# Kernel optimization log

Measured on AMD Instinct MI355X. Metric: run time of the kernel, lower is better.

Reference implementation:

```python
import jax, jax.numpy as jnp
import numpy as np

DIM = 512
N_GROUPS = 8
N_CODES = 1024
SUB = DIM // N_GROUPS
CB_LAMBDA = 1.0
COMMIT_LAMBDA = 0.25


def setup_inputs() -> dict:
    key = jax.random.key(0)
    k1, k2, k3 = jax.random.split(key, 3)
    x = jax.random.normal(k1, (8, DIM, 4096), dtype=jnp.float32)
    lim = 1.0 / N_CODES
    codebooks1 = jax.random.uniform(k2, (N_GROUPS, N_CODES, SUB), dtype=jnp.float32, minval=-lim, maxval=lim)
    codebooks2 = jax.random.uniform(k3, (N_GROUPS, N_CODES, SUB), dtype=jnp.float32, minval=-lim, maxval=lim)
    return {"x": x, "codebooks1": codebooks1, "codebooks2": codebooks2}


def _quantize_group(flat, cbs):
    # flat: (N, G, d), cbs: (G, K, d)
    x2 = jnp.sum(flat * flat, axis=-1, keepdims=True)          # (N, G, 1)
    e2 = jnp.sum(cbs * cbs, axis=-1)                            # (G, K)
    xe = jnp.einsum('ngd,gkd->ngk', flat, cbs)                  # (N, G, K)
    d = x2 + e2[None, :, :] - 2.0 * xe                          # (N, G, K)
    idx = jnp.argmin(d, axis=-1)                                # (N, G)
    z = cbs[jnp.arange(N_GROUPS)[None, :], idx]                 # (N, G, d)
    return z, idx


def reference(x, codebooks1, codebooks2):
    B, C, T = x.shape
    sg = jax.lax.stop_gradient
    # (B, C, T) -> (B*T, G, sub)
    xb = jnp.transpose(x, (0, 2, 1)).reshape(-1, N_GROUPS, SUB)
    residual = xb
    quantized = jnp.zeros_like(xb)
    losses = []
    all_indices = []
    for cbs in (codebooks1, codebooks2):
        z, idx = _quantize_group(residual, cbs)
        codebook_loss = jnp.mean((z - sg(residual)) ** 2)
        commit_loss = jnp.mean((sg(z) - residual) ** 2)
        losses.append(CB_LAMBDA * codebook_loss + COMMIT_LAMBDA * commit_loss)
        z_st = residual + sg(z - residual)  # straight-through
        residual = residual - z_st
        quantized = quantized + z_st
        all_indices.append(idx)
    total_loss = jnp.mean(jnp.stack(losses))
    quantized_out = jnp.transpose(quantized.reshape(B, T, C), (0, 2, 1))
    # indices in original order: layer-major, group-major -> (layers*G, B*T)
    indices = jnp.concatenate([idx.T for idx in all_indices], axis=0)
    return quantized_out, total_loss, indices
```

## Files before the change

### kernel.cpp

```cpp
#include <hip/hip_runtime.h>

#define GRP 8
#define SUBD 64
#define NCODE 1024
#define TLEN 4096
#define NBATCH 8
#define NVEC (NBATCH * TLEN)
#define QOUT (NBATCH * 512 * TLEN)
#define ROWS 128
#define NGRPS (NCODE / 8)

#define WS_E2   64
#define WS_IDX1 (WS_E2 + 65536)
#define WS_P1   (WS_IDX1 + 1048576)
#define WS_P2   (WS_P1 + 2097152)

typedef const __attribute__((address_space(1))) char GCHAR;
typedef __attribute__((address_space(3))) char LCHAR;
typedef float f2 __attribute__((ext_vector_type(2)));

__global__ __launch_bounds__(256) void k_e2(const float* __restrict__ cb1,
                                            const float* __restrict__ cb2,
                                            float* __restrict__ e2) {
    int i = blockIdx.x * 256 + threadIdx.x;
    const float* c = (i < GRP * NCODE) ? (cb1 + (size_t)i * SUBD)
                                       : (cb2 + (size_t)(i - GRP * NCODE) * SUBD);
    float s = 0.f;
#pragma unroll
    for (int d = 0; d < SUBD; ++d) s = __builtin_fmaf(c[d], c[d], s);
    e2[i] = s;
}

__global__ __launch_bounds__(256) void k_panel(const float* __restrict__ cb1,
                                               const float* __restrict__ cb2,
                                               float* __restrict__ cbP1,
                                               float* __restrict__ cbP2) {
    int i = blockIdx.x * 256 + threadIdx.x;
    int sel = i >> 13, rest = i & 8191, g = rest >> 10, k = rest & 1023;
    int grp = k >> 3, j = k & 7;
    const float* src = (sel ? cb2 : cb1) + ((size_t)g * NCODE + k) * SUBD;
    float* dst = (sel ? cbP2 : cbP1) + ((size_t)(g * NGRPS + grp) * SUBD) * 8 + j;
#pragma unroll
    for (int s = 0; s < 16; ++s) {
        float4 v = ((const float4*)src)[s];
#pragma unroll
        for (int dd = 0; dd < 4; ++dd) dst[(4 * s + dd) * 8] = ((const float*)&v)[dd];
    }
}

template <int STAGE2>
__global__ __launch_bounds__(256, 3) void k_vq(
    const float* __restrict__ x,
    const float* __restrict__ cb1,
    const float* __restrict__ cb2,
    const float* __restrict__ cbP,
    const float* __restrict__ e2,
    const int* __restrict__ idxPrev,
    int* __restrict__ idxOut,
    float* __restrict__ outIdxF,
    float* __restrict__ qout,
    double* __restrict__ lossAcc)
{
    __shared__ __align__(16) float xs[SUBD * ROWS];
    __shared__ float bdH[4 * ROWS];
    __shared__ int   biH[4 * ROWS];
    __shared__ int   i2s[ROWS];
    __shared__ double wsr[8];

    const int tid = threadIdx.x, w = tid >> 6, lane = tid & 63;
    const int g = blockIdx.y;
    const int row0 = blockIdx.x * ROWS;
    const int bz = row0 / TLEN, t0 = row0 % TLEN;
    const float* xsrc = x + ((size_t)(bz * 512 + g * SUBD)) * TLEN + t0;

    {
#pragma unroll
        for (int q = 0; q < 8; ++q) {
            int inst = w * 8 + q;
            int d = inst * 2 + (lane >> 5);
            const float* gp = xsrc + (size_t)d * TLEN + (lane & 31) * 4;
            float* lp = xs + inst * 256;
            __builtin_amdgcn_global_load_lds((GCHAR*)gp, (LCHAR*)lp, 16, 0, 0);
        }
    }
    __syncthreads();

    const int rowB = tid & 127, hi = tid >> 7;
    double ls1 = 0.0;
    int i1 = 0;
    if (STAGE2) {
        i1 = idxPrev[g * NVEC + row0 + rowB];
        const float4* z1v = (const float4*)(cb1 + ((size_t)g * NCODE + i1) * SUBD) + hi * 8;
#pragma unroll
        for (int s = 0; s < 8; ++s) {
            float4 z = z1v[s];
#pragma unroll
            for (int dd = 0; dd < 4; ++dd) {
                int d = hi * 32 + s * 4 + dd;
                float r = xs[d * ROWS + rowB];
                float zz = (&z.x)[dd];
                float tt = zz - r;
                float zst = r + tt;
                ls1 += (double)(tt * tt);
                float r2 = r - zst;
                xs[d * ROWS + rowB] = r2;
            }
        }
        __syncthreads();
    }

    const int w_u = __builtin_amdgcn_readfirstlane(w);
    const f2* xs2 = (const f2*)xs;

    f2 x2p = {0.f, 0.f};
#pragma unroll 8
    for (int d = 0; d < SUBD; ++d) {
        f2 rv = xs2[d * 64 + lane];
        x2p = __builtin_elementwise_fma(rv, rv, x2p);
    }
    const float x2a = x2p[0], x2b = x2p[1];

    const float* e2g = e2 + g * NCODE;
    float best[2] = {1e30f, 1e30f};
    int bidx[2] = {0, 0};

    for (int ib = 0; ib < 8; ++ib) {
        const float* cp = cbP + ((size_t)(g * NGRPS) + w_u * 32 + ib * 4) * (SUBD * 8);
        const float4* cb0 = (const float4*)(cp);
        const float4* cb1p = (const float4*)(cp + 1 * (SUBD * 8));
        const float4* cb2p = (const float4*)(cp + 2 * (SUBD * 8));
        const float4* cb3p = (const float4*)(cp + 3 * (SUBD * 8));
        f2 acc[2][4][4];
#pragma unroll
        for (int r = 0; r < 2; ++r)
#pragma unroll
            for (int gg = 0; gg < 4; ++gg)
#pragma unroll
                for (int p = 0; p < 4; ++p) acc[r][gg][p] = (f2){0.f, 0.f};

#pragma unroll 2
        for (int d = 0; d < SUBD; ++d) {
            f2 rv = xs2[d * 64 + lane];
            f2 xa2 = {rv[0], rv[0]}, xb2 = {rv[1], rv[1]};
            const float4* cbs[4] = {cb0, cb1p, cb2p, cb3p};
#pragma unroll
            for (int gg = 0; gg < 4; ++gg) {
                float4 q0 = cbs[gg][2 * d];
                float4 q1 = cbs[gg][2 * d + 1];
                f2 cv0 = {q0.x, q0.y}, cv1 = {q0.z, q0.w};
                f2 cv2 = {q1.x, q1.y}, cv3 = {q1.z, q1.w};
                acc[0][gg][0] = __builtin_elementwise_fma(xa2, cv0, acc[0][gg][0]);
                acc[0][gg][1] = __builtin_elementwise_fma(xa2, cv1, acc[0][gg][1]);
                acc[0][gg][2] = __builtin_elementwise_fma(xa2, cv2, acc[0][gg][2]);
                acc[0][gg][3] = __builtin_elementwise_fma(xa2, cv3, acc[0][gg][3]);
                acc[1][gg][0] = __builtin_elementwise_fma(xb2, cv0, acc[1][gg][0]);
                acc[1][gg][1] = __builtin_elementwise_fma(xb2, cv1, acc[1][gg][1]);
                acc[1][gg][2] = __builtin_elementwise_fma(xb2, cv2, acc[1][gg][2]);
                acc[1][gg][3] = __builtin_elementwise_fma(xb2, cv3, acc[1][gg][3]);
            }
        }

#pragma unroll
        for (int gg = 0; gg < 4; ++gg) {
            const float4* e4 = (const float4*)(e2g + w_u * 256 + ib * 32 + gg * 8);
            float4 e0 = e4[0], e1 = e4[1];
#pragma unroll
            for (int p = 0; p < 4; ++p) {
#pragma unroll
                for (int h = 0; h < 2; ++h) {
                    int j = 2 * p + h;
                    int k = w_u * 256 + ib * 32 + gg * 8 + j;
                    float ev = (j < 4) ? (&e0.x)[j] : (&e1.x)[j - 4];
                    float tva = x2a + ev;
                    float da = __builtin_fmaf(-2.0f, acc[0][gg][p][h], tva);
                    if (da < best[0]) { best[0] = da; bidx[0] = k; }
                    float tvb = x2b + ev;
                    float db = __builtin_fmaf(-2.0f, acc[1][gg][p][h], tvb);
                    if (db < best[1]) { best[1] = db; bidx[1] = k; }
                }
            }
        }
    }
    bdH[w * ROWS + 2 * lane]     = best[0];
    biH[w * ROWS + 2 * lane]     = bidx[0];
    bdH[w * ROWS + 2 * lane + 1] = best[1];
    biH[w * ROWS + 2 * lane + 1] = bidx[1];
    __syncthreads();

    if (tid < ROWS) {
        float bd = bdH[tid];
        int   bi = biH[tid];
#pragma unroll
        for (int wv = 1; wv < 4; ++wv) {
            float od = bdH[wv * ROWS + tid];
            int   oi = biH[wv * ROWS + tid];
            if (od < bd) { bd = od; bi = oi; }
        }
        int nv = row0 + tid;
        outIdxF[(size_t)g * NVEC + nv] = (float)bi;
        if (!STAGE2) idxOut[g * NVEC + nv] = bi;
        else i2s[tid] = bi;
    }

    double ls2 = 0.0;
    if (STAGE2) {
        __syncthreads();
        int bi = i2s[rowB];
        const float4* z1v = (const float4*)(cb1 + ((size_t)g * NCODE + i1) * SUBD) + hi * 8;
        const float4* z2v = (const float4*)(cb2 + ((size_t)g * NCODE + bi) * SUBD) + hi * 8;
        const float* xp = xsrc + rowB;
        float* op = qout + ((size_t)(bz * 512 + g * SUBD)) * TLEN + t0 + rowB;
#pragma unroll
        for (int s = 0; s < 8; ++s) {
            float4 z1 = z1v[s];
            float4 z2 = z2v[s];
#pragma unroll
            for (int dd = 0; dd < 4; ++dd) {
                int d = hi * 32 + s * 4 + dd;
                float xv = xp[(size_t)d * TLEN];
                float r2 = xs[d * ROWS + rowB];
                float z1f = (&z1.x)[dd];
                float z2f = (&z2.x)[dd];
                float t1 = z1f - xv;
                float zst1 = xv + t1;
                float t2 = z2f - r2;
                float zst2 = r2 + t2;
                float qv = zst1 + zst2;
                op[(size_t)d * TLEN] = qv;
                ls2 += (double)(t2 * t2);
            }
        }

#pragma unroll
        for (int off = 32; off; off >>= 1) {
            ls1 += __shfl_down(ls1, off, 64);
            ls2 += __shfl_down(ls2, off, 64);
        }
        if (lane == 0) { wsr[w] = ls1; wsr[4 + w] = ls2; }
        __syncthreads();
        if (tid == 0)
            atomicAdd(lossAcc + 0, wsr[0] + wsr[1] + wsr[2] + wsr[3]);
        else if (tid == 64)
            atomicAdd(lossAcc + 1, wsr[4] + wsr[5] + wsr[6] + wsr[7]);
    }
}

__global__ void k_final(float* __restrict__ lossOut, const double* __restrict__ lossAcc) {
    double m = (lossAcc[0] + lossAcc[1]) / (double)QOUT;
    lossOut[0] = (float)(0.625 * m);
}

extern "C" void kernel_launch(void* const* d_in, const int* in_sizes, int n_in,
                              void* d_out, int out_size, void* d_ws, size_t ws_size,
                              hipStream_t stream) {
    const float* x   = (const float*)d_in[0];
    const float* cb1 = (const float*)d_in[1];
    const float* cb2 = (const float*)d_in[2];
    float* out = (float*)d_out;

    char* ws = (char*)d_ws;
    double* lossAcc = (double*)ws;
    float* e2   = (float*)(ws + WS_E2);
    int*   idx1 = (int*)(ws + WS_IDX1);
    float* cbP1 = (float*)(ws + WS_P1);
    float* cbP2 = (float*)(ws + WS_P2);

    hipMemsetAsync(ws, 0, 16, stream);

    k_e2<<<dim3(64), dim3(256), 0, stream>>>(cb1, cb2, e2);
    k_panel<<<dim3(64), dim3(256), 0, stream>>>(cb1, cb2, cbP1, cbP2);

    dim3 grid(NVEC / ROWS, GRP);
    float* outIdx = out + QOUT + 1;
    k_vq<0><<<grid, dim3(256), 0, stream>>>(x, cb1, cb2, cbP1, e2,
                                            nullptr, idx1, outIdx, nullptr, nullptr);
    k_vq<1><<<grid, dim3(256), 0, stream>>>(x, cb1, cb2, cbP2, e2 + GRP * NCODE,
                                            idx1, nullptr, outIdx + (size_t)GRP * NVEC,
                                            out, lossAcc);
    k_final<<<1, 1, 0, stream>>>(out + QOUT, lossAcc);
}
```

Baseline: 795.2 us.

## Double rows per VQ block to 256 with 512 threads sharing codebook panels

Each VQ block now handles 256 rows with 8 waves. Two row-halves of waves scan the same codebook quarters, so each codebook panel fetch from global/L2 is reused across twice as many rows. The x tile load, LDS indexing, per-quarter min reduction and loss reduction are rewritten for the larger block. LDS use per block doubles and the grid halves, which can cut occupancy and the number of blocks available to fill the GPU.

```diff
diff --git a/kernel.cpp b/kernel.cpp
--- a/kernel.cpp
+++ b/kernel.cpp
@@ -7,7 +7,7 @@
 #define NBATCH 8
 #define NVEC (NBATCH * TLEN)
 #define QOUT (NBATCH * 512 * TLEN)
-#define ROWS 128
+#define ROWS 256
 #define NGRPS (NCODE / 8)
 
 #define WS_E2   64
@@ -49,7 +49,7 @@
 }
 
 template <int STAGE2>
-__global__ __launch_bounds__(256, 3) void k_vq(
+__global__ __launch_bounds__(512, 2) void k_vq(
     const float* __restrict__ x,
     const float* __restrict__ cb1,
     const float* __restrict__ cb2,
@@ -65,7 +65,7 @@
     __shared__ float bdH[4 * ROWS];
     __shared__ int   biH[4 * ROWS];
     __shared__ int   i2s[ROWS];
-    __shared__ double wsr[8];
+    __shared__ double wsr[16];
 
     const int tid = threadIdx.x, w = tid >> 6, lane = tid & 63;
     const int g = blockIdx.y;
@@ -75,17 +75,16 @@
 
     {
 #pragma unroll
-        for (int q = 0; q < 8; ++q) {
-            int inst = w * 8 + q;
-            int d = inst * 2 + (lane >> 5);
-            const float* gp = xsrc + (size_t)d * TLEN + (lane & 31) * 4;
-            float* lp = xs + inst * 256;
+        for (int qq = 0; qq < 8; ++qq) {
+            int d = w * 8 + qq;
+            const float* gp = xsrc + (size_t)d * TLEN + lane * 4;
+            float* lp = xs + d * 256;
             __builtin_amdgcn_global_load_lds((GCHAR*)gp, (LCHAR*)lp, 16, 0, 0);
         }
     }
     __syncthreads();
 
-    const int rowB = tid & 127, hi = tid >> 7;
+    const int rowB = tid & 255, hi = tid >> 8;
     double ls1 = 0.0;
     int i1 = 0;
     if (STAGE2) {
@@ -110,12 +109,14 @@
     }
 
     const int w_u = __builtin_amdgcn_readfirstlane(w);
+    const int h = w_u >> 2, q = w_u & 3;
+    const int pr = h * 64 + lane;
     const f2* xs2 = (const f2*)xs;
 
     f2 x2p = {0.f, 0.f};
 #pragma unroll 8
     for (int d = 0; d < SUBD; ++d) {
-        f2 rv = xs2[d * 64 + lane];
+        f2 rv = xs2[d * 128 + pr];
         x2p = __builtin_elementwise_fma(rv, rv, x2p);
     }
     const float x2a = x2p[0], x2b = x2p[1];
@@ -125,11 +126,11 @@
     int bidx[2] = {0, 0};
 
     for (int ib = 0; ib < 8; ++ib) {
-        const float* cp = cbP + ((size_t)(g * NGRPS) + w_u * 32 + ib * 4) * (SUBD * 8);
-        const float4* cb0 = (const float4*)(cp);
-        const float4* cb1p = (const float4*)(cp + 1 * (SUBD * 8));
-        const float4* cb2p = (const float4*)(cp + 2 * (SUBD * 8));
-        const float4* cb3p = (const float4*)(cp + 3 * (SUBD * 8));
+        const float* cp = cbP + ((size_t)(g * NGRPS) + q * 32 + ib * 4) * (SUBD * 8);
+        const float4* cbq0 = (const float4*)(cp);
+        const float4* cbq1 = (const float4*)(cp + 1 * (SUBD * 8));
+        const float4* cbq2 = (const float4*)(cp + 2 * (SUBD * 8));
+        const float4* cbq3 = (const float4*)(cp + 3 * (SUBD * 8));
         f2 acc[2][4][4];
 #pragma unroll
         for (int r = 0; r < 2; ++r)
@@ -140,9 +141,9 @@
 
 #pragma unroll 2
         for (int d = 0; d < SUBD; ++d) {
-            f2 rv = xs2[d * 64 + lane];
+            f2 rv = xs2[d * 128 + pr];
             f2 xa2 = {rv[0], rv[0]}, xb2 = {rv[1], rv[1]};
-            const float4* cbs[4] = {cb0, cb1p, cb2p, cb3p};
+            const float4* cbs[4] = {cbq0, cbq1, cbq2, cbq3};
 #pragma unroll
             for (int gg = 0; gg < 4; ++gg) {
                 float4 q0 = cbs[gg][2 * d];
@@ -162,38 +163,38 @@
 
 #pragma unroll
         for (int gg = 0; gg < 4; ++gg) {
-            const float4* e4 = (const float4*)(e2g + w_u * 256 + ib * 32 + gg * 8);
+            const float4* e4 = (const float4*)(e2g + q * 256 + ib * 32 + gg * 8);
             float4 e0 = e4[0], e1 = e4[1];
 #pragma unroll
             for (int p = 0; p < 4; ++p) {
 #pragma unroll
-                for (int h = 0; h < 2; ++h) {
-                    int j = 2 * p + h;
-                    int k = w_u * 256 + ib * 32 + gg * 8 + j;
+                for (int hh = 0; hh < 2; ++hh) {
+                    int j = 2 * p + hh;
+                    int k = q * 256 + ib * 32 + gg * 8 + j;
                     float ev = (j < 4) ? (&e0.x)[j] : (&e1.x)[j - 4];
                     float tva = x2a + ev;
-                    float da = __builtin_fmaf(-2.0f, acc[0][gg][p][h], tva);
+                    float da = __builtin_fmaf(-2.0f, acc[0][gg][p][hh], tva);
                     if (da < best[0]) { best[0] = da; bidx[0] = k; }
                     float tvb = x2b + ev;
-                    float db = __builtin_fmaf(-2.0f, acc[1][gg][p][h], tvb);
+                    float db = __builtin_fmaf(-2.0f, acc[1][gg][p][hh], tvb);
                     if (db < best[1]) { best[1] = db; bidx[1] = k; }
                 }
             }
         }
     }
-    bdH[w * ROWS + 2 * lane]     = best[0];
-    biH[w * ROWS + 2 * lane]     = bidx[0];
-    bdH[w * ROWS + 2 * lane + 1] = best[1];
-    biH[w * ROWS + 2 * lane + 1] = bidx[1];
+    bdH[q * ROWS + 2 * pr]     = best[0];
+    biH[q * ROWS + 2 * pr]     = bidx[0];
+    bdH[q * ROWS + 2 * pr + 1] = best[1];
+    biH[q * ROWS + 2 * pr + 1] = bidx[1];
     __syncthreads();
 
     if (tid < ROWS) {
         float bd = bdH[tid];
         int   bi = biH[tid];
 #pragma unroll
-        for (int wv = 1; wv < 4; ++wv) {
-            float od = bdH[wv * ROWS + tid];
-            int   oi = biH[wv * ROWS + tid];
+        for (int qv = 1; qv < 4; ++qv) {
+            float od = bdH[qv * ROWS + tid];
+            int   oi = biH[qv * ROWS + tid];
             if (od < bd) { bd = od; bi = oi; }
         }
         int nv = row0 + tid;
@@ -225,8 +226,8 @@
                 float zst1 = xv + t1;
                 float t2 = z2f - r2;
                 float zst2 = r2 + t2;
-                float qv = zst1 + zst2;
-                op[(size_t)d * TLEN] = qv;
+                float qv2 = zst1 + zst2;
+                op[(size_t)d * TLEN] = qv2;
                 ls2 += (double)(t2 * t2);
             }
         }
@@ -236,12 +237,19 @@
             ls1 += __shfl_down(ls1, off, 64);
             ls2 += __shfl_down(ls2, off, 64);
         }
-        if (lane == 0) { wsr[w] = ls1; wsr[4 + w] = ls2; }
+        if (lane == 0) { wsr[w] = ls1; wsr[8 + w] = ls2; }
         __syncthreads();
-        if (tid == 0)
-            atomicAdd(lossAcc + 0, wsr[0] + wsr[1] + wsr[2] + wsr[3]);
-        else if (tid == 64)
-            atomicAdd(lossAcc + 1, wsr[4] + wsr[5] + wsr[6] + wsr[7]);
+        if (tid == 0) {
+            double s = 0.0;
+#pragma unroll
+            for (int i = 0; i < 8; ++i) s += wsr[i];
+            atomicAdd(lossAcc + 0, s);
+        } else if (tid == 64) {
+            double s = 0.0;
+#pragma unroll
+            for (int i = 0; i < 8; ++i) s += wsr[8 + i];
+            atomicAdd(lossAcc + 1, s);
+        }
     }
 }
 
@@ -272,9 +280,9 @@
 
     dim3 grid(NVEC / ROWS, GRP);
     float* outIdx = out + QOUT + 1;
-    k_vq<0><<<grid, dim3(256), 0, stream>>>(x, cb1, cb2, cbP1, e2,
+    k_vq<0><<<grid, dim3(512), 0, stream>>>(x, cb1, cb2, cbP1, e2,
                                             nullptr, idx1, outIdx, nullptr, nullptr);
-    k_vq<1><<<grid, dim3(256), 0, stream>>>(x, cb1, cb2, cbP2, e2 + GRP * NCODE,
+    k_vq<1><<<grid, dim3(512), 0, stream>>>(x, cb1, cb2, cbP2, e2 + GRP * NCODE,
                                             idx1, nullptr, outIdx + (size_t)GRP * NVEC,
                                             out, lossAcc);
     k_final<<<1, 1, 0, stream>>>(out + QOUT, lossAcc);
```

After: 851.5 us. 1.07x slower.

## Fuse both VQ stages into one kernel and merge codebook prep kernels

Applied to the files above, without the earlier changes.

Both residual quantization stages now run in a single kernel. The residual stays in shared memory between stages instead of x being reloaded and stage-1 indices going through global memory. The e2 norm and panel-layout prep kernels are merged into one launch. This removes one full read of x, the idx round trip and two launches. The cost is a longer kernel with extra barriers, and register pressure may change.

```diff
diff --git a/kernel.cpp b/kernel.cpp
--- a/kernel.cpp
+++ b/kernel.cpp
@@ -11,107 +11,43 @@
 #define NGRPS (NCODE / 8)
 
 #define WS_E2   64
-#define WS_IDX1 (WS_E2 + 65536)
-#define WS_P1   (WS_IDX1 + 1048576)
+#define WS_P1   (WS_E2 + 65536)
 #define WS_P2   (WS_P1 + 2097152)
 
 typedef const __attribute__((address_space(1))) char GCHAR;
 typedef __attribute__((address_space(3))) char LCHAR;
 typedef float f2 __attribute__((ext_vector_type(2)));
 
-__global__ __launch_bounds__(256) void k_e2(const float* __restrict__ cb1,
-                                            const float* __restrict__ cb2,
-                                            float* __restrict__ e2) {
-    int i = blockIdx.x * 256 + threadIdx.x;
-    const float* c = (i < GRP * NCODE) ? (cb1 + (size_t)i * SUBD)
-                                       : (cb2 + (size_t)(i - GRP * NCODE) * SUBD);
-    float s = 0.f;
-#pragma unroll
-    for (int d = 0; d < SUBD; ++d) s = __builtin_fmaf(c[d], c[d], s);
-    e2[i] = s;
-}
-
-__global__ __launch_bounds__(256) void k_panel(const float* __restrict__ cb1,
-                                               const float* __restrict__ cb2,
-                                               float* __restrict__ cbP1,
-                                               float* __restrict__ cbP2) {
+__global__ __launch_bounds__(256) void k_prep(const float* __restrict__ cb1,
+                                              const float* __restrict__ cb2,
+                                              float* __restrict__ e2,
+                                              float* __restrict__ cbP1,
+                                              float* __restrict__ cbP2) {
     int i = blockIdx.x * 256 + threadIdx.x;
     int sel = i >> 13, rest = i & 8191, g = rest >> 10, k = rest & 1023;
     int grp = k >> 3, j = k & 7;
     const float* src = (sel ? cb2 : cb1) + ((size_t)g * NCODE + k) * SUBD;
     float* dst = (sel ? cbP2 : cbP1) + ((size_t)(g * NGRPS + grp) * SUBD) * 8 + j;
-#pragma unroll
-    for (int s = 0; s < 16; ++s) {
-        float4 v = ((const float4*)src)[s];
-#pragma unroll
-        for (int dd = 0; dd < 4; ++dd) dst[(4 * s + dd) * 8] = ((const float*)&v)[dd];
-    }
-}
-
-template <int STAGE2>
-__global__ __launch_bounds__(256, 3) void k_vq(
-    const float* __restrict__ x,
-    const float* __restrict__ cb1,
-    const float* __restrict__ cb2,
-    const float* __restrict__ cbP,
-    const float* __restrict__ e2,
-    const int* __restrict__ idxPrev,
-    int* __restrict__ idxOut,
-    float* __restrict__ outIdxF,
-    float* __restrict__ qout,
-    double* __restrict__ lossAcc)
+    float s = 0.f;
+#pragma unroll
+    for (int ss = 0; ss < 16; ++ss) {
+        float4 v = ((const float4*)src)[ss];
+#pragma unroll
+        for (int dd = 0; dd < 4; ++dd) {
+            float c = ((const float*)&v)[dd];
+            s = __builtin_fmaf(c, c, s);
+            dst[(4 * ss + dd) * 8] = c;
+        }
+    }
+    e2[i] = s;
+}
+
+__device__ __forceinline__ void scan_quarter(
+    const f2* __restrict__ xs2, int lane, int w_u,
+    const float* __restrict__ cbPg,
+    const float* __restrict__ e2g,
+    float& bd0, int& bi0, float& bd1, int& bi1)
 {
-    __shared__ __align__(16) float xs[SUBD * ROWS];
-    __shared__ float bdH[4 * ROWS];
-    __shared__ int   biH[4 * ROWS];
-    __shared__ int   i2s[ROWS];
-    __shared__ double wsr[8];
-
-    const int tid = threadIdx.x, w = tid >> 6, lane = tid & 63;
-    const int g = blockIdx.y;
-    const int row0 = blockIdx.x * ROWS;
-    const int bz = row0 / TLEN, t0 = row0 % TLEN;
-    const float* xsrc = x + ((size_t)(bz * 512 + g * SUBD)) * TLEN + t0;
-
-    {
-#pragma unroll
-        for (int q = 0; q < 8; ++q) {
-            int inst = w * 8 + q;
-            int d = inst * 2 + (lane >> 5);
-            const float* gp = xsrc + (size_t)d * TLEN + (lane & 31) * 4;
-            float* lp = xs + inst * 256;
-            __builtin_amdgcn_global_load_lds((GCHAR*)gp, (LCHAR*)lp, 16, 0, 0);
-        }
-    }
-    __syncthreads();
-
-    const int rowB = tid & 127, hi = tid >> 7;
-    double ls1 = 0.0;
-    int i1 = 0;
-    if (STAGE2) {
-        i1 = idxPrev[g * NVEC + row0 + rowB];
-        const float4* z1v = (const float4*)(cb1 + ((size_t)g * NCODE + i1) * SUBD) + hi * 8;
-#pragma unroll
-        for (int s = 0; s < 8; ++s) {
-            float4 z = z1v[s];
-#pragma unroll
-            for (int dd = 0; dd < 4; ++dd) {
-                int d = hi * 32 + s * 4 + dd;
-                float r = xs[d * ROWS + rowB];
-                float zz = (&z.x)[dd];
-                float tt = zz - r;
-                float zst = r + tt;
-                ls1 += (double)(tt * tt);
-                float r2 = r - zst;
-                xs[d * ROWS + rowB] = r2;
-            }
-        }
-        __syncthreads();
-    }
-
-    const int w_u = __builtin_amdgcn_readfirstlane(w);
-    const f2* xs2 = (const f2*)xs;
-
     f2 x2p = {0.f, 0.f};
 #pragma unroll 8
     for (int d = 0; d < SUBD; ++d) {
@@ -120,16 +56,15 @@
     }
     const float x2a = x2p[0], x2b = x2p[1];
 
-    const float* e2g = e2 + g * NCODE;
     float best[2] = {1e30f, 1e30f};
     int bidx[2] = {0, 0};
 
     for (int ib = 0; ib < 8; ++ib) {
-        const float* cp = cbP + ((size_t)(g * NGRPS) + w_u * 32 + ib * 4) * (SUBD * 8);
-        const float4* cb0 = (const float4*)(cp);
-        const float4* cb1p = (const float4*)(cp + 1 * (SUBD * 8));
-        const float4* cb2p = (const float4*)(cp + 2 * (SUBD * 8));
-        const float4* cb3p = (const float4*)(cp + 3 * (SUBD * 8));
+        const float* cp = cbPg + (size_t)(w_u * 32 + ib * 4) * (SUBD * 8);
+        const float4* cq0 = (const float4*)(cp);
+        const float4* cq1 = (const float4*)(cp + 1 * (SUBD * 8));
+        const float4* cq2 = (const float4*)(cp + 2 * (SUBD * 8));
+        const float4* cq3 = (const float4*)(cp + 3 * (SUBD * 8));
         f2 acc[2][4][4];
 #pragma unroll
         for (int r = 0; r < 2; ++r)
@@ -142,7 +77,7 @@
         for (int d = 0; d < SUBD; ++d) {
             f2 rv = xs2[d * 64 + lane];
             f2 xa2 = {rv[0], rv[0]}, xb2 = {rv[1], rv[1]};
-            const float4* cbs[4] = {cb0, cb1p, cb2p, cb3p};
+            const float4* cbs[4] = {cq0, cq1, cq2, cq3};
 #pragma unroll
             for (int gg = 0; gg < 4; ++gg) {
                 float4 q0 = cbs[gg][2 * d];
@@ -181,10 +116,61 @@
             }
         }
     }
-    bdH[w * ROWS + 2 * lane]     = best[0];
-    biH[w * ROWS + 2 * lane]     = bidx[0];
-    bdH[w * ROWS + 2 * lane + 1] = best[1];
-    biH[w * ROWS + 2 * lane + 1] = bidx[1];
+    bd0 = best[0]; bi0 = bidx[0];
+    bd1 = best[1]; bi1 = bidx[1];
+}
+
+__global__ __launch_bounds__(256, 3) void k_vq(
+    const float* __restrict__ x,
+    const float* __restrict__ cb1,
+    const float* __restrict__ cb2,
+    const float* __restrict__ cbP1,
+    const float* __restrict__ cbP2,
+    const float* __restrict__ e2,
+    float* __restrict__ outIdxF,
+    float* __restrict__ qout,
+    double* __restrict__ lossAcc)
+{
+    __shared__ __align__(16) float xs[SUBD * ROWS];
+    __shared__ float bdH[4 * ROWS];
+    __shared__ int   biH[4 * ROWS];
+    __shared__ int   i1s[ROWS];
+    __shared__ int   i2s[ROWS];
+    __shared__ double wsr[8];
+
+    const int tid = threadIdx.x, w = tid >> 6, lane = tid & 63;
+    const int g = blockIdx.y;
+    const int row0 = blockIdx.x * ROWS;
+    const int bz = row0 / TLEN, t0 = row0 % TLEN;
+    const float* xsrc = x + ((size_t)(bz * 512 + g * SUBD)) * TLEN + t0;
+
+    {
+#pragma unroll
+        for (int q = 0; q < 8; ++q) {
+            int inst = w * 8 + q;
+            int d = inst * 2 + (lane >> 5);
+            const float* gp = xsrc + (size_t)d * TLEN + (lane & 31) * 4;
+            float* lp = xs + inst * 256;
+            __builtin_amdgcn_global_load_lds((GCHAR*)gp, (LCHAR*)lp, 16, 0, 0);
+        }
+    }
+    __syncthreads();
+
+    const int w_u = __builtin_amdgcn_readfirstlane(w);
+    const f2* xs2 = (const f2*)xs;
+    const float* cbP1g = cbP1 + (size_t)g * (NGRPS * SUBD * 8);
+    const float* cbP2g = cbP2 + (size_t)g * (NGRPS * SUBD * 8);
+    const float* e2g1 = e2 + g * NCODE;
+    const float* e2g2 = e2 + GRP * NCODE + g * NCODE;
+
+    {
+        float bd0, bd1; int bi0, bi1;
+        scan_quarter(xs2, lane, w_u, cbP1g, e2g1, bd0, bi0, bd1, bi1);
+        bdH[w * ROWS + 2 * lane]     = bd0;
+        biH[w * ROWS + 2 * lane]     = bi0;
+        bdH[w * ROWS + 2 * lane + 1] = bd1;
+        biH[w * ROWS + 2 * lane + 1] = bi1;
+    }
     __syncthreads();
 
     if (tid < ROWS) {
@@ -198,13 +184,60 @@
         }
         int nv = row0 + tid;
         outIdxF[(size_t)g * NVEC + nv] = (float)bi;
-        if (!STAGE2) idxOut[g * NVEC + nv] = bi;
-        else i2s[tid] = bi;
-    }
+        i1s[tid] = bi;
+    }
+    __syncthreads();
+
+    const int rowB = tid & 127, hi = tid >> 7;
+    double ls1 = 0.0;
+    const int i1 = i1s[rowB];
+    {
+        const float4* z1v = (const float4*)(cb1 + ((size_t)g * NCODE + i1) * SUBD) + hi * 8;
+#pragma unroll
+        for (int s = 0; s < 8; ++s) {
+            float4 z = z1v[s];
+#pragma unroll
+            for (int dd = 0; dd < 4; ++dd) {
+                int d = hi * 32 + s * 4 + dd;
+                float r = xs[d * ROWS + rowB];
+                float zz = (&z.x)[dd];
+                float tt = zz - r;
+                float zst = r + tt;
+                ls1 += (double)(tt * tt);
+                float r2 = r - zst;
+                xs[d * ROWS + rowB] = r2;
+            }
+        }
+    }
+    __syncthreads();
+
+    {
+        float bd0, bd1; int bi0, bi1;
+        scan_quarter(xs2, lane, w_u, cbP2g, e2g2, bd0, bi0, bd1, bi1);
+        bdH[w * ROWS + 2 * lane]     = bd0;
+        biH[w * ROWS + 2 * lane]     = bi0;
+        bdH[w * ROWS + 2 * lane + 1] = bd1;
+        biH[w * ROWS + 2 * lane + 1] = bi1;
+    }
+    __syncthreads();
+
+    if (tid < ROWS) {
+        float bd = bdH[tid];
+        int   bi = biH[tid];
+#pragma unroll
+        for (int wv = 1; wv < 4; ++wv) {
+            float od = bdH[wv * ROWS + tid];
+            int   oi = biH[wv * ROWS + tid];
+            if (od < bd) { bd = od; bi = oi; }
+        }
+        int nv = row0 + tid;
+        outIdxF[(size_t)(GRP + g) * NVEC + nv] = (float)bi;
+        i2s[tid] = bi;
+    }
+    __syncthreads();
 
     double ls2 = 0.0;
-    if (STAGE2) {
-        __syncthreads();
+    {
         int bi = i2s[rowB];
         const float4* z1v = (const float4*)(cb1 + ((size_t)g * NCODE + i1) * SUBD) + hi * 8;
         const float4* z2v = (const float4*)(cb2 + ((size_t)g * NCODE + bi) * SUBD) + hi * 8;
@@ -230,19 +263,19 @@
                 ls2 += (double)(t2 * t2);
             }
         }
-
-#pragma unroll
-        for (int off = 32; off; off >>= 1) {
-            ls1 += __shfl_down(ls1, off, 64);
-            ls2 += __shfl_down(ls2, off, 64);
-        }
-        if (lane == 0) { wsr[w] = ls1; wsr[4 + w] = ls2; }
-        __syncthreads();
-        if (tid == 0)
-            atomicAdd(lossAcc + 0, wsr[0] + wsr[1] + wsr[2] + wsr[3]);
-        else if (tid == 64)
-            atomicAdd(lossAcc + 1, wsr[4] + wsr[5] + wsr[6] + wsr[7]);
-    }
+    }
+
+#pragma unroll
+    for (int off = 32; off; off >>= 1) {
+        ls1 += __shfl_down(ls1, off, 64);
+        ls2 += __shfl_down(ls2, off, 64);
+    }
+    if (lane == 0) { wsr[w] = ls1; wsr[4 + w] = ls2; }
+    __syncthreads();
+    if (tid == 0)
+        atomicAdd(lossAcc + 0, wsr[0] + wsr[1] + wsr[2] + wsr[3]);
+    else if (tid == 64)
+        atomicAdd(lossAcc + 1, wsr[4] + wsr[5] + wsr[6] + wsr[7]);
 }
 
 __global__ void k_final(float* __restrict__ lossOut, const double* __restrict__ lossAcc) {
@@ -261,21 +294,16 @@
     char* ws = (char*)d_ws;
     double* lossAcc = (double*)ws;
     float* e2   = (float*)(ws + WS_E2);
-    int*   idx1 = (int*)(ws + WS_IDX1);
     float* cbP1 = (float*)(ws + WS_P1);
     float* cbP2 = (float*)(ws + WS_P2);
 
     hipMemsetAsync(ws, 0, 16, stream);
 
-    k_e2<<<dim3(64), dim3(256), 0, stream>>>(cb1, cb2, e2);
-    k_panel<<<dim3(64), dim3(256), 0, stream>>>(cb1, cb2, cbP1, cbP2);
+    k_prep<<<dim3(64), dim3(256), 0, stream>>>(cb1, cb2, e2, cbP1, cbP2);
 
     dim3 grid(NVEC / ROWS, GRP);
     float* outIdx = out + QOUT + 1;
-    k_vq<0><<<grid, dim3(256), 0, stream>>>(x, cb1, cb2, cbP1, e2,
-                                            nullptr, idx1, outIdx, nullptr, nullptr);
-    k_vq<1><<<grid, dim3(256), 0, stream>>>(x, cb1, cb2, cbP2, e2 + GRP * NCODE,
-                                            idx1, nullptr, outIdx + (size_t)GRP * NVEC,
-                                            out, lossAcc);
+    k_vq<<<grid, dim3(256), 0, stream>>>(x, cb1, cb2, cbP1, cbP2, e2,
+                                         outIdx, out, lossAcc);
     k_final<<<1, 1, 0, stream>>>(out + QOUT, lossAcc);
 }
```

Result: no change. 788.8 us (-0.8%).

## Use packed min for argmin and recompute winning chunk's index afterward

Applied to the files above, without the earlier changes.

Merges the codebook norm and panel-layout prep kernels into one launch. In the main VQ kernel, the per-code compare-and-select argmin is replaced by packed f2 min reductions that only track which 32-code chunk held the minimum. After the cross-wave reduction, one thread per row recomputes distances over that 32-code chunk to recover the exact index. This cuts the select/compare work in the hot loop but adds extra syncs, a serial 64x32 recompute per row on half the threads, and a 64-float register array that may raise register pressure. Ties are broken by lowest chunk and lowest index, and recomputed distances must match the first pass bit-for-bit for the argmin to stay consistent.

```diff
diff --git a/kernel.cpp b/kernel.cpp
--- a/kernel.cpp
+++ b/kernel.cpp
@@ -19,33 +19,35 @@
 typedef __attribute__((address_space(3))) char LCHAR;
 typedef float f2 __attribute__((ext_vector_type(2)));
 
-__global__ __launch_bounds__(256) void k_e2(const float* __restrict__ cb1,
-                                            const float* __restrict__ cb2,
-                                            float* __restrict__ e2) {
-    int i = blockIdx.x * 256 + threadIdx.x;
-    const float* c = (i < GRP * NCODE) ? (cb1 + (size_t)i * SUBD)
-                                       : (cb2 + (size_t)(i - GRP * NCODE) * SUBD);
-    float s = 0.f;
-#pragma unroll
-    for (int d = 0; d < SUBD; ++d) s = __builtin_fmaf(c[d], c[d], s);
-    e2[i] = s;
-}
-
-__global__ __launch_bounds__(256) void k_panel(const float* __restrict__ cb1,
-                                               const float* __restrict__ cb2,
-                                               float* __restrict__ cbP1,
-                                               float* __restrict__ cbP2) {
+static __device__ __forceinline__ f2 f2min(f2 a, f2 b) {
+    f2 r;
+    r[0] = __builtin_fminf(a[0], b[0]);
+    r[1] = __builtin_fminf(a[1], b[1]);
+    return r;
+}
+
+__global__ __launch_bounds__(256) void k_prep(const float* __restrict__ cb1,
+                                              const float* __restrict__ cb2,
+                                              float* __restrict__ e2,
+                                              float* __restrict__ cbP1,
+                                              float* __restrict__ cbP2) {
     int i = blockIdx.x * 256 + threadIdx.x;
     int sel = i >> 13, rest = i & 8191, g = rest >> 10, k = rest & 1023;
     int grp = k >> 3, j = k & 7;
     const float* src = (sel ? cb2 : cb1) + ((size_t)g * NCODE + k) * SUBD;
     float* dst = (sel ? cbP2 : cbP1) + ((size_t)(g * NGRPS + grp) * SUBD) * 8 + j;
-#pragma unroll
-    for (int s = 0; s < 16; ++s) {
-        float4 v = ((const float4*)src)[s];
-#pragma unroll
-        for (int dd = 0; dd < 4; ++dd) dst[(4 * s + dd) * 8] = ((const float*)&v)[dd];
-    }
+    float s = 0.f;
+#pragma unroll
+    for (int ss = 0; ss < 16; ++ss) {
+        float4 v = ((const float4*)src)[ss];
+#pragma unroll
+        for (int dd = 0; dd < 4; ++dd) {
+            float c = ((const float*)&v)[dd];
+            s = __builtin_fmaf(c, c, s);
+            dst[(4 * ss + dd) * 8] = c;
+        }
+    }
+    e2[i] = s;
 }
 
 template <int STAGE2>
@@ -64,6 +66,7 @@
     __shared__ __align__(16) float xs[SUBD * ROWS];
     __shared__ float bdH[4 * ROWS];
     __shared__ int   biH[4 * ROWS];
+    __shared__ float mG[ROWS];
     __shared__ int   i2s[ROWS];
     __shared__ double wsr[8];
 
@@ -118,18 +121,19 @@
         f2 rv = xs2[d * 64 + lane];
         x2p = __builtin_elementwise_fma(rv, rv, x2p);
     }
-    const float x2a = x2p[0], x2b = x2p[1];
+    const f2 x2a2 = {x2p[0], x2p[0]}, x2b2 = {x2p[1], x2p[1]};
+    const f2 n2 = {-2.0f, -2.0f};
 
     const float* e2g = e2 + g * NCODE;
-    float best[2] = {1e30f, 1e30f};
-    int bidx[2] = {0, 0};
+    float m0 = 1e30f, m1 = 1e30f;
+    int ib0 = 0, ib1 = 0;
 
     for (int ib = 0; ib < 8; ++ib) {
         const float* cp = cbP + ((size_t)(g * NGRPS) + w_u * 32 + ib * 4) * (SUBD * 8);
-        const float4* cb0 = (const float4*)(cp);
-        const float4* cb1p = (const float4*)(cp + 1 * (SUBD * 8));
-        const float4* cb2p = (const float4*)(cp + 2 * (SUBD * 8));
-        const float4* cb3p = (const float4*)(cp + 3 * (SUBD * 8));
+        const float4* cq0 = (const float4*)(cp);
+        const float4* cq1 = (const float4*)(cp + 1 * (SUBD * 8));
+        const float4* cq2 = (const float4*)(cp + 2 * (SUBD * 8));
+        const float4* cq3 = (const float4*)(cp + 3 * (SUBD * 8));
         f2 acc[2][4][4];
 #pragma unroll
         for (int r = 0; r < 2; ++r)
@@ -142,7 +146,7 @@
         for (int d = 0; d < SUBD; ++d) {
             f2 rv = xs2[d * 64 + lane];
             f2 xa2 = {rv[0], rv[0]}, xb2 = {rv[1], rv[1]};
-            const float4* cbs[4] = {cb0, cb1p, cb2p, cb3p};
+            const float4* cbs[4] = {cq0, cq1, cq2, cq3};
 #pragma unroll
             for (int gg = 0; gg < 4; ++gg) {
                 float4 q0 = cbs[gg][2 * d];
@@ -160,42 +164,95 @@
             }
         }
 
+        f2 cmA = {1e30f, 1e30f}, cmB = {1e30f, 1e30f};
 #pragma unroll
         for (int gg = 0; gg < 4; ++gg) {
             const float4* e4 = (const float4*)(e2g + w_u * 256 + ib * 32 + gg * 8);
             float4 e0 = e4[0], e1 = e4[1];
+            f2 ep[4] = {{e0.x, e0.y}, {e0.z, e0.w}, {e1.x, e1.y}, {e1.z, e1.w}};
 #pragma unroll
             for (int p = 0; p < 4; ++p) {
-#pragma unroll
-                for (int h = 0; h < 2; ++h) {
-                    int j = 2 * p + h;
-                    int k = w_u * 256 + ib * 32 + gg * 8 + j;
-                    float ev = (j < 4) ? (&e0.x)[j] : (&e1.x)[j - 4];
-                    float tva = x2a + ev;
-                    float da = __builtin_fmaf(-2.0f, acc[0][gg][p][h], tva);
-                    if (da < best[0]) { best[0] = da; bidx[0] = k; }
-                    float tvb = x2b + ev;
-                    float db = __builtin_fmaf(-2.0f, acc[1][gg][p][h], tvb);
-                    if (db < best[1]) { best[1] = db; bidx[1] = k; }
-                }
-            }
-        }
-    }
-    bdH[w * ROWS + 2 * lane]     = best[0];
-    biH[w * ROWS + 2 * lane]     = bidx[0];
-    bdH[w * ROWS + 2 * lane + 1] = best[1];
-    biH[w * ROWS + 2 * lane + 1] = bidx[1];
+                f2 tva = x2a2 + ep[p];
+                f2 da = __builtin_elementwise_fma(n2, acc[0][gg][p], tva);
+                cmA = f2min(cmA, da);
+                f2 tvb = x2b2 + ep[p];
+                f2 db = __builtin_elementwise_fma(n2, acc[1][gg][p], tvb);
+                cmB = f2min(cmB, db);
+            }
+        }
+        float cA = __builtin_fminf(cmA[0], cmA[1]);
+        float cB = __builtin_fminf(cmB[0], cmB[1]);
+        if (cA < m0) { m0 = cA; ib0 = ib; }
+        if (cB < m1) { m1 = cB; ib1 = ib; }
+    }
+    bdH[w * ROWS + 2 * lane]     = m0;
+    bdH[w * ROWS + 2 * lane + 1] = m1;
     __syncthreads();
 
     if (tid < ROWS) {
-        float bd = bdH[tid];
-        int   bi = biH[tid];
+        float m = bdH[tid];
+#pragma unroll
+        for (int wv = 1; wv < 4; ++wv) m = __builtin_fminf(m, bdH[wv * ROWS + tid]);
+        mG[tid] = m;
+    }
+    __syncthreads();
+
+    {
+        float g0 = mG[2 * lane], g1 = mG[2 * lane + 1];
+        biH[w * ROWS + 2 * lane]     = (m0 == g0) ? (w_u * 16 + ib0) : 4096;
+        biH[w * ROWS + 2 * lane + 1] = (m1 == g1) ? (w_u * 16 + ib1) : 4096;
+    }
+    __syncthreads();
+
+    if (tid < ROWS) {
+        int c = biH[tid];
 #pragma unroll
         for (int wv = 1; wv < 4; ++wv) {
-            float od = bdH[wv * ROWS + tid];
-            int   oi = biH[wv * ROWS + tid];
-            if (od < bd) { bd = od; bi = oi; }
-        }
+            int o = biH[wv * ROWS + tid];
+            if (o < c) c = o;
+        }
+        int wstar = c >> 4, ibstar = c & 15;
+
+        float xr[64];
+#pragma unroll
+        for (int d = 0; d < SUBD; ++d) xr[d] = xs[d * ROWS + tid];
+        float x2r = 0.f;
+#pragma unroll
+        for (int d = 0; d < SUBD; ++d) x2r = __builtin_fmaf(xr[d], xr[d], x2r);
+
+        int kbase = wstar * 256 + ibstar * 32;
+        const float* cpR = cbP + ((size_t)(g * NGRPS) + wstar * 32 + ibstar * 4) * (SUBD * 8);
+        float best = 1e30f;
+        int bj = 0;
+#pragma unroll
+        for (int gg = 0; gg < 4; ++gg) {
+            const float4* c4 = (const float4*)(cpR + gg * (SUBD * 8));
+            float a8[8];
+#pragma unroll
+            for (int j = 0; j < 8; ++j) a8[j] = 0.f;
+#pragma unroll 4
+            for (int d = 0; d < SUBD; ++d) {
+                float4 q0 = c4[2 * d];
+                float4 q1 = c4[2 * d + 1];
+                float xv = xr[d];
+                a8[0] = __builtin_fmaf(xv, q0.x, a8[0]);
+                a8[1] = __builtin_fmaf(xv, q0.y, a8[1]);
+                a8[2] = __builtin_fmaf(xv, q0.z, a8[2]);
+                a8[3] = __builtin_fmaf(xv, q0.w, a8[3]);
+                a8[4] = __builtin_fmaf(xv, q1.x, a8[4]);
+                a8[5] = __builtin_fmaf(xv, q1.y, a8[5]);
+                a8[6] = __builtin_fmaf(xv, q1.z, a8[6]);
+                a8[7] = __builtin_fmaf(xv, q1.w, a8[7]);
+            }
+#pragma unroll
+            for (int j = 0; j < 8; ++j) {
+                int kk = kbase + gg * 8 + j;
+                float tv = x2r + e2g[kk];
+                float dist = __builtin_fmaf(-2.0f, a8[j], tv);
+                if (dist < best) { best = dist; bj = gg * 8 + j; }
+            }
+        }
+        int bi = kbase + bj;
         int nv = row0 + tid;
         outIdxF[(size_t)g * NVEC + nv] = (float)bi;
         if (!STAGE2) idxOut[g * NVEC + nv] = bi;
@@ -267,8 +324,7 @@
 
     hipMemsetAsync(ws, 0, 16, stream);
 
-    k_e2<<<dim3(64), dim3(256), 0, stream>>>(cb1, cb2, e2);
-    k_panel<<<dim3(64), dim3(256), 0, stream>>>(cb1, cb2, cbP1, cbP2);
+    k_prep<<<dim3(64), dim3(256), 0, stream>>>(cb1, cb2, e2, cbP1, cbP2);
 
     dim3 grid(NVEC / ROWS, GRP);
     float* outIdx = out + QOUT + 1;
```

Result: slower. 1.078 ms (+35.5%).
